# Kernel optimization log

Measured on AMD Instinct MI355X. Metric: run time of the kernel, lower is better.

Reference implementation:

```python
import jax, jax.numpy as jnp
import numpy as np

# Dims: batch N, time T, joints V=9, K=5 adjacency partitions (spatial strategy, max_hop=2),
# in channels 16, out channels = coords = 3, temporal kernel 9 (ConvTranspose, stride 1, pad 4).
N, T, V, C_IN, C_OUT, K, KT = 256, 2048, 9, 16, 3, 5, 9


def setup_inputs() -> dict:
    key = jax.random.key(0)
    ks = jax.random.split(key, 6)
    pose_feats = jax.random.normal(ks[0], (N, T, V * C_IN), jnp.float32)
    # Fixed (non-trainable) multi-partition normalized adjacency A2: [K, V, V].
    # Graph values come from ted_db constants in the repo; stand-in: row-normalized random.
    A = jax.random.uniform(ks[1], (K, V, V), jnp.float32)
    A = A / jnp.sum(A, axis=-1, keepdims=True)
    # GCN 1x1 conv: in -> K*C_OUT channels
    W_gcn = jax.random.normal(ks[2], (K, C_OUT, C_IN), jnp.float32) * (1.0 / np.sqrt(C_IN))
    b_gcn = jax.random.normal(ks[3], (K, C_OUT), jnp.float32) * 0.02
    # Temporal ConvTranspose2d(C_OUT, C_OUT, kernel=(9,1), stride=(1,1), padding=(4,0));
    # torch weight layout [in, out, kH, kW]
    W_tcn = jax.random.normal(ks[4], (C_OUT, C_OUT, KT, 1), jnp.float32) * (1.0 / np.sqrt(C_OUT * KT))
    b_tcn = jax.random.normal(ks[5], (C_OUT,), jnp.float32) * 0.02
    return {"pose_feats": pose_feats, "A": A, "W_gcn": W_gcn, "b_gcn": b_gcn,
            "W_tcn": W_tcn, "b_tcn": b_tcn}


def _st_gcn_transpose(x, A, W_gcn, b_gcn, W_tcn, b_tcn):
    # x: [n, c_in, t, v]
    # 1x1 conv to K*C_OUT channels, then adjacency contraction over partitions k
    y = jnp.einsum('nctv,koc->nkotv', x, W_gcn) + b_gcn[None, :, :, None, None]
    y = jnp.einsum('nkotv,kvw->notw', y, A)  # [n, c_out, t, v]
    # temporal transposed conv, kernel (9,1), stride 1, torch padding 4 -> jax pad (4,4)
    y = jax.lax.conv_transpose(y, W_tcn, strides=(1, 1), padding=[(4, 4), (0, 0)],
                               dimension_numbers=('NCHW', 'IOHW', 'NCHW'),
                               transpose_kernel=True)
    y = y + b_tcn[None, :, None, None]
    return jax.nn.leaky_relu(y, 0.01)


def reference(pose_feats, A, W_gcn, b_gcn, W_tcn, b_tcn):
    n, t, f = pose_feats.shape
    x = pose_feats.reshape(n, t, V, C_IN).transpose(0, 3, 1, 2)  # [n, c_in, t, v]
    y = _st_gcn_transpose(x, A, W_gcn, b_gcn, W_tcn, b_tcn)      # [n, c_out, t, v]
    return y.transpose(0, 2, 3, 1).reshape(n, t, V * C_OUT)       # [n, t, 27]
```

## Files before the change

kernel.cpp:

```cpp
#include <hip/hip_runtime.h>

typedef short short8 __attribute__((ext_vector_type(8)));
typedef float f32x4  __attribute__((ext_vector_type(4)));

constexpr int N_    = 256;
constexpr int T_    = 2048;
constexpr int V_    = 9;
constexpr int FIN_  = 144;
constexpr int J_    = 27;
constexpr int KT_   = 9;
constexpr int THREADS_ = 256;
constexpr int TILE_ = 248;
constexpr int NTILE_ = 9;
constexpr int ZROWS_ = 256;
constexpr int ZS_ = 28;
constexpr int ZBUF_B = ZROWS_ * ZS_ * 4;

constexpr int BF_OFF_F = 0;
constexpr int B0_OFF   = 2560;
constexpr int WT_OFF   = 2587;
constexpr int BT_OFF   = 2668;

__device__ __forceinline__ unsigned short bf16_rne(float x) {
    unsigned u = __float_as_uint(x);
    u = (u + 0x7FFFu + ((u >> 16) & 1u)) >> 16;
    return (unsigned short)u;
}
__device__ __forceinline__ unsigned pk2(float a, float b) {
    return (unsigned)bf16_rne(a) | ((unsigned)bf16_rne(b) << 16);
}

__global__ void setup_weights(const float* __restrict__ A,
                              const float* __restrict__ Wg,
                              const float* __restrict__ bg,
                              const float* __restrict__ Wt_in,
                              const float* __restrict__ bt,
                              float* __restrict__ ws) {
    __shared__ float Wc[FIN_ * J_];
    const int tid = threadIdx.x;
    for (int idx = tid; idx < FIN_ * J_; idx += 256) {
        const int f = idx / J_, j = idx % J_;
        const int v = f >> 4, c = f & 15;
        const int w = j / 3, o = j % 3;
        float s = 0.f;
        #pragma unroll
        for (int k = 0; k < 5; ++k)
            s += Wg[(k * 3 + o) * 16 + c] * A[(k * 9 + v) * 9 + w];
        Wc[idx] = s;
    }
    __syncthreads();
    unsigned short* bfp = (unsigned short*)(ws + BF_OFF_F);
    for (int i = tid; i < 5120; i += 256) {
        const int e = i & 7, lane = (i >> 3) & 63, nt = (i >> 9) & 1, s = i >> 10;
        const int k = s * 32 + (lane >> 4) * 8 + e;
        const int n = nt * 16 + (lane & 15);
        const float val = (k < FIN_ && n < J_) ? Wc[k * J_ + n] : 0.f;
        bfp[i] = bf16_rne(val);
    }
    if (tid < J_) {
        const int w = tid / 3, o = tid % 3;
        float s = 0.f;
        #pragma unroll
        for (int k = 0; k < 5; ++k) {
            float cs = 0.f;
            #pragma unroll
            for (int v = 0; v < V_; ++v) cs += A[(k * 9 + v) * 9 + w];
            s += bg[k * 3 + o] * cs;
        }
        ws[B0_OFF + tid] = s;
    }
    if (tid < 81) {
        const int o = tid / 27, r = tid % 27, o2 = r / 9, dd = r % 9;
        ws[WT_OFF + tid] = Wt_in[(o2 * 3 + o) * 9 + (8 - dd)];
    }
    if (tid < 3) ws[BT_OFF + tid] = bt[tid];
}

__global__ __launch_bounds__(THREADS_) void fused_stgcn(const float* __restrict__ pose,
                                                        const float* __restrict__ cw,
                                                        float* __restrict__ out) {
    __shared__ __align__(16) float zbuf[ZROWS_ * ZS_];

    const int tid  = threadIdx.x;
    const int bid  = blockIdx.x;
    const int nb   = bid / NTILE_;
    const int tile = bid % NTILE_;
    const int t0   = tile * TILE_;
    const int lane = tid & 63;
    const int wv   = tid >> 6;
    const int g8   = lane >> 4;
    const int j0   = lane & 15;

    short8 bfrag[5][2];
    {
        const short8* bsrc = (const short8*)(cw + BF_OFF_F);
        #pragma unroll
        for (int s = 0; s < 5; ++s)
            #pragma unroll
            for (int nt = 0; nt < 2; ++nt)
                bfrag[s][nt] = bsrc[(s * 2 + nt) * 64 + lane];
    }
    const float b0n0 = cw[B0_OFF + j0];
    const float b0n1 = (j0 < 11) ? cw[B0_OFF + 16 + j0] : 0.f;

    const size_t nrow0 = (size_t)nb * T_;

    float4 pA[5], pB[5];
    auto issue = [&](int mt, float4* Av, float4* Bv) {
        const int text = t0 - 4 + wv * 64 + mt * 16 + j0;
        const bool okr = (text >= 0 && text < T_);
        const float* rowp = pose + (nrow0 + (okr ? text : 0)) * FIN_;
        #pragma unroll
        for (int s = 0; s < 5; ++s) {
            const int k0 = s * 32 + g8 * 8;
            const bool ok = okr && (k0 < FIN_);
            Av[s] = ok ? *(const float4*)(rowp + k0)     : make_float4(0.f, 0.f, 0.f, 0.f);
            Bv[s] = ok ? *(const float4*)(rowp + k0 + 4) : make_float4(0.f, 0.f, 0.f, 0.f);
        }
    };

    issue(0, pA, pB);
    #pragma unroll
    for (int mt = 0; mt < 4; ++mt) {
        short8 af[5];
        #pragma unroll
        for (int s = 0; s < 5; ++s) {
            union { unsigned u[4]; short8 s8; } cvu;
            cvu.u[0] = pk2(pA[s].x, pA[s].y);
            cvu.u[1] = pk2(pA[s].z, pA[s].w);
            cvu.u[2] = pk2(pB[s].x, pB[s].y);
            cvu.u[3] = pk2(pB[s].z, pB[s].w);
            af[s] = cvu.s8;
        }
        if (mt < 3) issue(mt + 1, pA, pB);

        f32x4 acc0 = {0.f, 0.f, 0.f, 0.f};
        f32x4 acc1 = {0.f, 0.f, 0.f, 0.f};
        #pragma unroll
        for (int s = 0; s < 5; ++s) {
            acc0 = __builtin_amdgcn_mfma_f32_16x16x32_bf16(af[s], bfrag[s][0], acc0, 0, 0, 0);
            acc1 = __builtin_amdgcn_mfma_f32_16x16x32_bf16(af[s], bfrag[s][1], acc1, 0, 0, 0);
        }
        #pragma unroll
        for (int r = 0; r < 4; ++r) {
            const int zrow = wv * 64 + mt * 16 + g8 * 4 + r;
            const int text = t0 - 4 + zrow;
            const bool okz = (text >= 0 && text < T_);
            zbuf[zrow * ZS_ + j0] = okz ? acc0[r] + b0n0 : 0.f;
            if (j0 < 11)
                zbuf[zrow * ZS_ + 16 + j0] = okz ? acc1[r] + b0n1 : 0.f;
        }
    }
    __syncthreads();

    const int rows_out = min(TILE_, T_ - t0);
    float oacc[J_];
    if (tid < rows_out) {
        #pragma unroll
        for (int w = 0; w < V_; ++w)
            #pragma unroll
            for (int o2 = 0; o2 < 3; ++o2)
                oacc[w * 3 + o2] = cw[BT_OFF + o2];
        #pragma unroll
        for (int dd = 0; dd < KT_; ++dd) {
            union { f32x4 v4[7]; float f[28]; } zu;
            const f32x4* zp = (const f32x4*)&zbuf[(tid + dd) * ZS_];
            #pragma unroll
            for (int c = 0; c < 7; ++c) zu.v4[c] = zp[c];
            #pragma unroll
            for (int o = 0; o < 3; ++o) {
                #pragma unroll
                for (int o2 = 0; o2 < 3; ++o2) {
                    const float wt = cw[WT_OFF + o * 27 + o2 * 9 + dd];
                    #pragma unroll
                    for (int w = 0; w < V_; ++w)
                        oacc[w * 3 + o2] = fmaf(zu.f[w * 3 + o], wt, oacc[w * 3 + o2]);
                }
            }
        }
        #pragma unroll
        for (int j = 0; j < J_; ++j) oacc[j] = fmaxf(oacc[j], 0.01f * oacc[j]);
    }
    __syncthreads();
    if (tid < rows_out) {
        #pragma unroll
        for (int j = 0; j < J_; ++j) zbuf[tid * J_ + j] = oacc[j];
    }
    __syncthreads();

    const int total4 = (rows_out * J_) / 4;
    float4* dst4 = (float4*)(out + (nrow0 + t0) * J_);
    const float4* src4 = (const float4*)zbuf;
    for (int idx = tid; idx < total4; idx += THREADS_)
        dst4[idx] = src4[idx];
}

extern "C" void kernel_launch(void* const* d_in, const int* in_sizes, int n_in,
                              void* d_out, int out_size, void* d_ws, size_t ws_size,
                              hipStream_t stream) {
    const float* pose = (const float*)d_in[0];
    const float* A    = (const float*)d_in[1];
    const float* Wg   = (const float*)d_in[2];
    const float* bg   = (const float*)d_in[3];
    const float* Wt   = (const float*)d_in[4];
    const float* bt   = (const float*)d_in[5];
    float* ws   = (float*)d_ws;
    float* outp = (float*)d_out;

    setup_weights<<<1, 256, 0, stream>>>(A, Wg, bg, Wt, bt, ws);
    fused_stgcn<<<N_ * NTILE_, THREADS_, 0, stream>>>(pose, ws, outp);
}
```

Measured before the change: 87.24 us.

## Stage pose rows through LDS with coalesced loads and double-buffered register prefetch

Pose input is now loaded cooperatively: each thread fetches contiguous float4 chunks across 64-row blocks, converts them to bf16, and writes them into a padded LDS tile. The MFMA A-fragments are then read from LDS instead of being gathered per lane straight from global memory. The next 64-row block is prefetched into a second register set while the current one is staged. Each step adds barriers and about 21KB of extra LDS, and launch bounds ask for 3 blocks per CU, which may limit occupancy or force register spills.

```diff
diff --git a/kernel.cpp b/kernel.cpp
--- a/kernel.cpp
+++ b/kernel.cpp
@@ -10,11 +10,13 @@
 constexpr int J_    = 27;
 constexpr int KT_   = 9;
 constexpr int THREADS_ = 256;
-constexpr int TILE_ = 248;
+constexpr int TILE_  = 248;
 constexpr int NTILE_ = 9;
-constexpr int ZROWS_ = 256;
-constexpr int ZS_ = 28;
-constexpr int ZBUF_B = ZROWS_ * ZS_ * 4;
+constexpr int XSTRIDE_B = 336;
+constexpr int XBUF_B  = 64 * XSTRIDE_B;
+constexpr int ZROWS_  = 256;
+constexpr int ZS_     = 28;
+constexpr int SMEM_B  = XBUF_B + ZROWS_ * ZS_ * 4;
 
 constexpr int BF_OFF_F = 0;
 constexpr int B0_OFF   = 2560;
@@ -76,10 +78,11 @@
     if (tid < 3) ws[BT_OFF + tid] = bt[tid];
 }
 
-__global__ __launch_bounds__(THREADS_) void fused_stgcn(const float* __restrict__ pose,
-                                                        const float* __restrict__ cw,
-                                                        float* __restrict__ out) {
-    __shared__ __align__(16) float zbuf[ZROWS_ * ZS_];
+__global__ __launch_bounds__(THREADS_, 3) void fused_stgcn(const float* __restrict__ pose,
+                                                           const float* __restrict__ cw,
+                                                           float* __restrict__ out) {
+    __shared__ __align__(16) unsigned char smem[SMEM_B];
+    float* zbuf = (float*)(smem + XBUF_B);
 
     const int tid  = threadIdx.x;
     const int bid  = blockIdx.x;
@@ -90,7 +93,44 @@
     const int wv   = tid >> 6;
     const int g8   = lane >> 4;
     const int j0   = lane & 15;
-
+    const size_t nrow0 = (size_t)nb * T_;
+
+    auto WB = []() {
+        asm volatile("s_waitcnt lgkmcnt(0)" ::: "memory");
+        __builtin_amdgcn_s_barrier();
+        asm volatile("" ::: "memory");
+    };
+
+    auto issue = [&](int h, float4* ld) {
+        #pragma unroll
+        for (int q = 0; q < 9; ++q) {
+            const int fidx = q * THREADS_ + tid;
+            const int r = fidx / 36, c4 = fidx % 36;
+            const int text = t0 - 4 + h * 64 + r;
+            const bool ok = (text >= 0 && text < T_);
+            const float* p = pose + (nrow0 + (size_t)(ok ? text : 0)) * FIN_ + c4 * 4;
+            ld[q] = ok ? *(const float4*)p : make_float4(0.f, 0.f, 0.f, 0.f);
+        }
+    };
+    auto stage = [&](const float4* ld) {
+        #pragma unroll
+        for (int q = 0; q < 9; ++q) {
+            const int fidx = q * THREADS_ + tid;
+            const int r = fidx / 36, c4 = fidx % 36;
+            uint2 u;
+            u.x = pk2(ld[q].x, ld[q].y);
+            u.y = pk2(ld[q].z, ld[q].w);
+            *(uint2*)(smem + r * XSTRIDE_B + c4 * 8) = u;
+        }
+    };
+
+    float4 lda[9], ldb[9];
+    issue(0, lda);
+
+    for (int i = tid; i < 512; i += THREADS_) {
+        const int r = i >> 3, w = i & 7;
+        *(float*)(smem + r * XSTRIDE_B + 288 + w * 4) = 0.f;
+    }
     short8 bfrag[5][2];
     {
         const short8* bsrc = (const short8*)(cw + BF_OFF_F);
@@ -103,55 +143,34 @@
     const float b0n0 = cw[B0_OFF + j0];
     const float b0n1 = (j0 < 11) ? cw[B0_OFF + 16 + j0] : 0.f;
 
-    const size_t nrow0 = (size_t)nb * T_;
-
-    float4 pA[5], pB[5];
-    auto issue = [&](int mt, float4* Av, float4* Bv) {
-        const int text = t0 - 4 + wv * 64 + mt * 16 + j0;
-        const bool okr = (text >= 0 && text < T_);
-        const float* rowp = pose + (nrow0 + (okr ? text : 0)) * FIN_;
-        #pragma unroll
-        for (int s = 0; s < 5; ++s) {
-            const int k0 = s * 32 + g8 * 8;
-            const bool ok = okr && (k0 < FIN_);
-            Av[s] = ok ? *(const float4*)(rowp + k0)     : make_float4(0.f, 0.f, 0.f, 0.f);
-            Bv[s] = ok ? *(const float4*)(rowp + k0 + 4) : make_float4(0.f, 0.f, 0.f, 0.f);
-        }
-    };
-
-    issue(0, pA, pB);
     #pragma unroll
-    for (int mt = 0; mt < 4; ++mt) {
-        short8 af[5];
-        #pragma unroll
-        for (int s = 0; s < 5; ++s) {
-            union { unsigned u[4]; short8 s8; } cvu;
-            cvu.u[0] = pk2(pA[s].x, pA[s].y);
-            cvu.u[1] = pk2(pA[s].z, pA[s].w);
-            cvu.u[2] = pk2(pB[s].x, pB[s].y);
-            cvu.u[3] = pk2(pB[s].z, pB[s].w);
-            af[s] = cvu.s8;
-        }
-        if (mt < 3) issue(mt + 1, pA, pB);
-
+    for (int h = 0; h < 4; ++h) {
+        float4* cur = (h & 1) ? ldb : lda;
+        float4* nxt = (h & 1) ? lda : ldb;
+        if (h < 3) issue(h + 1, nxt);
+        stage(cur);
+        WB();
+
+        const unsigned char* abase = smem + (wv * 16 + j0) * XSTRIDE_B;
         f32x4 acc0 = {0.f, 0.f, 0.f, 0.f};
         f32x4 acc1 = {0.f, 0.f, 0.f, 0.f};
         #pragma unroll
         for (int s = 0; s < 5; ++s) {
-            acc0 = __builtin_amdgcn_mfma_f32_16x16x32_bf16(af[s], bfrag[s][0], acc0, 0, 0, 0);
-            acc1 = __builtin_amdgcn_mfma_f32_16x16x32_bf16(af[s], bfrag[s][1], acc1, 0, 0, 0);
+            const short8 af = *(const short8*)(abase + s * 64 + g8 * 16);
+            acc0 = __builtin_amdgcn_mfma_f32_16x16x32_bf16(af, bfrag[s][0], acc0, 0, 0, 0);
+            acc1 = __builtin_amdgcn_mfma_f32_16x16x32_bf16(af, bfrag[s][1], acc1, 0, 0, 0);
         }
         #pragma unroll
         for (int r = 0; r < 4; ++r) {
-            const int zrow = wv * 64 + mt * 16 + g8 * 4 + r;
+            const int zrow = h * 64 + wv * 16 + g8 * 4 + r;
             const int text = t0 - 4 + zrow;
             const bool okz = (text >= 0 && text < T_);
             zbuf[zrow * ZS_ + j0] = okz ? acc0[r] + b0n0 : 0.f;
             if (j0 < 11)
                 zbuf[zrow * ZS_ + 16 + j0] = okz ? acc1[r] + b0n1 : 0.f;
         }
-    }
-    __syncthreads();
+        WB();
+    }
 
     const int rows_out = min(TILE_, T_ - t0);
     float oacc[J_];
@@ -181,12 +200,12 @@
         #pragma unroll
         for (int j = 0; j < J_; ++j) oacc[j] = fmaxf(oacc[j], 0.01f * oacc[j]);
     }
-    __syncthreads();
+    WB();
     if (tid < rows_out) {
         #pragma unroll
         for (int j = 0; j < J_; ++j) zbuf[tid * J_ + j] = oacc[j];
     }
-    __syncthreads();
+    WB();
 
     const int total4 = (rows_out * J_) / 4;
     float4* dst4 = (float4*)(out + (nrow0 + t0) * J_);
```

Result: no change. 87.69 us (+0.5%).
